# Optimization experiments

Measured on AMD Instinct MI355X. Metric: run time of the kernel, lower is better.

Reference implementation:

```python
import jax, jax.numpy as jnp
import numpy as np

SCALE = 100.0  # scale_up in logsumexp_pool


def setup_inputs() -> dict:
    key = jax.random.key(0)
    # NHWC, channels_last
    x = jax.random.normal(key, (8, 256, 256, 64), dtype=jnp.float32)
    return {"x": x}


def reference(x):
    # Faithful to logsumexp_pool: transpose NHWC -> [C,H,W,N], scale by 100,
    # extract 2x2 stride-2 VALID patches (depth axis = 2*2*N after transpose,
    # so the logsumexp reduces over the window AND the batch dim), descale,
    # expand_dims + transpose -> output [1, H/2, W/2, C].
    N, H, W, C = x.shape
    t = jnp.transpose(x, (3, 1, 2, 0)) * SCALE          # [C, H, W, N]
    # stride 2, kernel 2, VALID padding, even H/W -> non-overlapping windows;
    t = t.reshape(C, H // 2, 2, W // 2, 2, N)
    r = jax.nn.logsumexp(t, axis=(2, 4, 5)) * (1.0 / SCALE)  # [C, H/2, W/2]
    return jnp.transpose(r[..., None], (3, 1, 2, 0))    # [1, H/2, W/2, C]
```

## Files before the change

kernel.cpp:

```cpp
#include <hip/hip_runtime.h>


constexpr float SCALE = 100.0f;
constexpr float INV_SCALE = 0.01f;

__global__ __launch_bounds__(256, 6) void lse_pool_kernel(const float* __restrict__ x,
                                                          float* __restrict__ out) {
    const int t   = blockIdx.x * 256 + threadIdx.x;
    const int cg  = t & 15;
    const int pix = t >> 4;
    const int wo  = pix & 127;
    const int ho  = pix >> 7;
    const int c   = cg << 2;
    const int h0  = ho << 1;
    const int w0  = wo << 1;

    const size_t NSTRIDE = (size_t)256 * 256 * 64;
    const float* p = x + ((size_t)h0 * 256 + (size_t)w0) * 64 + (size_t)c;

    float m[4], s[4];
#pragma unroll
    for (int j = 0; j < 4; ++j) { m[j] = -1e30f; s[j] = 0.0f; }

#pragma unroll
    for (int np = 0; np < 4; ++np) {
        float4 v[8];
#pragma unroll
        for (int k = 0; k < 8; ++k) {
            const int n  = (np << 1) | (k >> 2);
            const int dh = (k >> 1) & 1;
            const int dw = k & 1;
            v[k] = *reinterpret_cast<const float4*>(
                p + (size_t)n * NSTRIDE + (size_t)(dh * 256 + dw) * 64);
        }

        float cm[4] = { v[0].x, v[0].y, v[0].z, v[0].w };
#pragma unroll
        for (int k = 1; k < 8; ++k) {
            cm[0] = fmaxf(cm[0], v[k].x);
            cm[1] = fmaxf(cm[1], v[k].y);
            cm[2] = fmaxf(cm[2], v[k].z);
            cm[3] = fmaxf(cm[3], v[k].w);
        }

        float cs[4] = { 0.f, 0.f, 0.f, 0.f };
#pragma unroll
        for (int k = 0; k < 8; ++k) {
            cs[0] += __expf((v[k].x - cm[0]) * SCALE);
            cs[1] += __expf((v[k].y - cm[1]) * SCALE);
            cs[2] += __expf((v[k].z - cm[2]) * SCALE);
            cs[3] += __expf((v[k].w - cm[3]) * SCALE);
        }

#pragma unroll
        for (int j = 0; j < 4; ++j) {
            const float mn = fmaxf(m[j], cm[j]);
            s[j] = s[j] * __expf((m[j] - mn) * SCALE)
                 + cs[j] * __expf((cm[j] - mn) * SCALE);
            m[j] = mn;
        }
    }

    float4 r;
    r.x = m[0] + __logf(s[0]) * INV_SCALE;
    r.y = m[1] + __logf(s[1]) * INV_SCALE;
    r.z = m[2] + __logf(s[2]) * INV_SCALE;
    r.w = m[3] + __logf(s[3]) * INV_SCALE;

    *reinterpret_cast<float4*>(out + (size_t)pix * 64 + (size_t)c) = r;
}

extern "C" void kernel_launch(void* const* d_in, const int* in_sizes, int n_in,
                              void* d_out, int out_size, void* d_ws, size_t ws_size,
                              hipStream_t stream) {
    const float* x = (const float*)d_in[0];
    float* out = (float*)d_out;
    lse_pool_kernel<<<1024, 256, 0, stream>>>(x, out);
}
```

Before: 184.9 us.

## Split each pooling window across four lanes and combine with warp shuffles

```diff
diff --git a/kernel.cpp b/kernel.cpp
--- a/kernel.cpp
+++ b/kernel.cpp
@@ -4,70 +4,69 @@
 constexpr float SCALE = 100.0f;
 constexpr float INV_SCALE = 0.01f;
 
-__global__ __launch_bounds__(256, 6) void lse_pool_kernel(const float* __restrict__ x,
+__global__ __launch_bounds__(256, 8) void lse_pool_kernel(const float* __restrict__ x,
                                                           float* __restrict__ out) {
     const int t   = blockIdx.x * 256 + threadIdx.x;
     const int cg  = t & 15;
-    const int pix = t >> 4;
+    const int dw  = (t >> 4) & 1;
+    const int nh  = (t >> 5) & 1;
+    const int pix = t >> 6;
     const int wo  = pix & 127;
     const int ho  = pix >> 7;
-    const int c   = cg << 2;
-    const int h0  = ho << 1;
-    const int w0  = wo << 1;
 
     const size_t NSTRIDE = (size_t)256 * 256 * 64;
-    const float* p = x + ((size_t)h0 * 256 + (size_t)w0) * 64 + (size_t)c;
+    const size_t ROW     = (size_t)256 * 64;
 
-    float m[4], s[4];
+    const float* p = x + ((size_t)(ho << 1) * 256 + (size_t)((wo << 1) | dw)) * 64
+                       + (size_t)(cg << 2)
+                       + (size_t)nh * 4 * NSTRIDE;
+
+    float4 v[8];
 #pragma unroll
-    for (int j = 0; j < 4; ++j) { m[j] = -1e30f; s[j] = 0.0f; }
+    for (int k = 0; k < 8; ++k) {
+        v[k] = *reinterpret_cast<const float4*>(p + (size_t)(k >> 1) * NSTRIDE
+                                                  + (size_t)(k & 1) * ROW);
+    }
+
+    float m[4] = { v[0].x, v[0].y, v[0].z, v[0].w };
+#pragma unroll
+    for (int k = 1; k < 8; ++k) {
+        m[0] = fmaxf(m[0], v[k].x);
+        m[1] = fmaxf(m[1], v[k].y);
+        m[2] = fmaxf(m[2], v[k].z);
+        m[3] = fmaxf(m[3], v[k].w);
+    }
+
+    float s[4] = { 0.f, 0.f, 0.f, 0.f };
+#pragma unroll
+    for (int k = 0; k < 8; ++k) {
+        s[0] += __expf((v[k].x - m[0]) * SCALE);
+        s[1] += __expf((v[k].y - m[1]) * SCALE);
+        s[2] += __expf((v[k].z - m[2]) * SCALE);
+        s[3] += __expf((v[k].w - m[3]) * SCALE);
+    }
 
 #pragma unroll
-    for (int np = 0; np < 4; ++np) {
-        float4 v[8];
-#pragma unroll
-        for (int k = 0; k < 8; ++k) {
-            const int n  = (np << 1) | (k >> 2);
-            const int dh = (k >> 1) & 1;
-            const int dw = k & 1;
-            v[k] = *reinterpret_cast<const float4*>(
-                p + (size_t)n * NSTRIDE + (size_t)(dh * 256 + dw) * 64);
-        }
-
-        float cm[4] = { v[0].x, v[0].y, v[0].z, v[0].w };
-#pragma unroll
-        for (int k = 1; k < 8; ++k) {
-            cm[0] = fmaxf(cm[0], v[k].x);
-            cm[1] = fmaxf(cm[1], v[k].y);
-            cm[2] = fmaxf(cm[2], v[k].z);
-            cm[3] = fmaxf(cm[3], v[k].w);
-        }
-
-        float cs[4] = { 0.f, 0.f, 0.f, 0.f };
-#pragma unroll
-        for (int k = 0; k < 8; ++k) {
-            cs[0] += __expf((v[k].x - cm[0]) * SCALE);
-            cs[1] += __expf((v[k].y - cm[1]) * SCALE);
-            cs[2] += __expf((v[k].z - cm[2]) * SCALE);
-            cs[3] += __expf((v[k].w - cm[3]) * SCALE);
-        }
-
+    for (int bit = 16; bit <= 32; bit <<= 1) {
 #pragma unroll
         for (int j = 0; j < 4; ++j) {
-            const float mn = fmaxf(m[j], cm[j]);
+            const float mo = __shfl_xor(m[j], bit);
+            const float so = __shfl_xor(s[j], bit);
+            const float mn = fmaxf(m[j], mo);
             s[j] = s[j] * __expf((m[j] - mn) * SCALE)
-                 + cs[j] * __expf((cm[j] - mn) * SCALE);
+                 + so   * __expf((mo   - mn) * SCALE);
             m[j] = mn;
         }
     }
 
-    float4 r;
-    r.x = m[0] + __logf(s[0]) * INV_SCALE;
-    r.y = m[1] + __logf(s[1]) * INV_SCALE;
-    r.z = m[2] + __logf(s[2]) * INV_SCALE;
-    r.w = m[3] + __logf(s[3]) * INV_SCALE;
-
-    *reinterpret_cast<float4*>(out + (size_t)pix * 64 + (size_t)c) = r;
+    if ((t & 48) == 0) {
+        float4 r;
+        r.x = m[0] + __logf(s[0]) * INV_SCALE;
+        r.y = m[1] + __logf(s[1]) * INV_SCALE;
+        r.z = m[2] + __logf(s[2]) * INV_SCALE;
+        r.w = m[3] + __logf(s[3]) * INV_SCALE;
+        *reinterpret_cast<float4*>(out + (size_t)pix * 64 + (size_t)(cg << 2)) = r;
+    }
 }
 
 extern "C" void kernel_launch(void* const* d_in, const int* in_sizes, int n_in,
@@ -75,5 +74,5 @@
                               hipStream_t stream) {
     const float* x = (const float*)d_in[0];
     float* out = (float*)d_out;
-    lse_pool_kernel<<<1024, 256, 0, stream>>>(x, out);
+    lse_pool_kernel<<<4096, 256, 0, stream>>>(x, out);
 }
```

Measured after the change: 187.5 us. Within noise of the previous version (+1.4%).
